# Performance work log

Measured on AMD Instinct MI355X. Metric: run time of the kernel, lower is better.

The kernel has to match this reference:

```python
import jax, jax.numpy as jnp
import numpy as np


def _pairwise_sq_dist(x, y):
    # x: [B, N, 3], y: [B, M, 3] -> P: [B, N, M] squared Euclidean distances
    xx = jnp.sum(x * x, axis=-1)                      # [B, N]
    yy = jnp.sum(y * y, axis=-1)                      # [B, M]
    zz = jnp.einsum('bnd,bmd->bnm', x, y)             # [B, N, M]
    return xx[:, :, None] + yy[:, None, :] - 2.0 * zz


def setup_inputs() -> dict:
    key = jax.random.key(0)
    k1, k2 = jax.random.split(key)
    B, K = 8, 8192
    adv_pc = jax.random.normal(k1, (B, K, 3), dtype=jnp.float32)
    ori_pc = jax.random.normal(k2, (B, K, 3), dtype=jnp.float32)
    weights = jnp.ones((B,), dtype=jnp.float32)
    return {"adv_pc": adv_pc, "ori_pc": ori_pc, "weights": weights}


def reference(adv_pc, ori_pc, weights):
    # P = pairwise_dist(gts=ori_pc, preds=adv_pc): [B, N_ori, N_adv]
    P = _pairwise_sq_dist(ori_pc, adv_pc)
    # method='adv2ori': loss1 = max over adv points of min over ori points
    loss1 = jnp.max(jnp.min(P, axis=1), axis=1)       # [B]
    loss = loss1 * weights
    return jnp.mean(loss)                             # batch_avg=True
```

## Files before the change

kernel.cpp:

```cpp
#include <hip/hip_runtime.h>


#define KPTS 8192
#define BATCH 8
#define NSPLIT 8
#define RBLK (KPTS / NSPLIT)
#define TSLICE (RBLK / 32)
#define CBLK 512
#define MCHUNK (KPTS / CBLK)

typedef _Float16 half8 __attribute__((ext_vector_type(8)));
typedef float f32x16 __attribute__((ext_vector_type(16)));

__device__ __forceinline__ float min16acc(float rm, const f32x16 c) {
    float u0 = fminf(fminf(c[0],  c[1]),  c[2]);
    float u1 = fminf(fminf(c[3],  c[4]),  c[5]);
    float u2 = fminf(fminf(c[6],  c[7]),  c[8]);
    float u3 = fminf(fminf(c[9],  c[10]), c[11]);
    float u4 = fminf(fminf(c[12], c[13]), c[14]);
    float u5 = fminf(fminf(u0, u1), c[15]);
    float u6 = fminf(fminf(u2, u3), u4);
    return fminf(fminf(u5, u6), rm);
}

__global__ __launch_bounds__(256) void hausdorff(const float* __restrict__ adv,
                                                 const float* __restrict__ ori,
                                                 float* __restrict__ part,
                                                 float* __restrict__ out) {
    __shared__ _Float16 sA[(TSLICE + 1) * 512];

    const int bid  = blockIdx.x;
    const int b    = bid >> 7;
    const int mc   = (bid >> 3) & (MCHUNK - 1);
    const int ns   = bid & 7;
    const int tid  = threadIdx.x;
    const int lane = tid & 63;
    const int wv   = tid >> 6;
    const int r    = lane & 31;
    const int hk   = lane >> 5;

    if (bid == 0 && tid == 0) out[0] = 0.0f;

    const _Float16 Z = (_Float16)0.0f, ONE = (_Float16)1.0f;

    const float* advb = adv + (size_t)b * KPTS * 3;
    const int m0 = mc * CBLK + wv * 128 + r;
    half8 bf0, bf1, bf2, bf3;
    float aa0, aa1, aa2, aa3;
#pragma unroll
    for (int i = 0; i < 4; ++i) {
        const int m = m0 + 32 * i;
        float ax = advb[3 * m], ay = advb[3 * m + 1], az = advb[3 * m + 2];
        float aa = ax * ax + ay * ay + az * az;
        float tx = -2.f * ax, ty = -2.f * ay, tz = -2.f * az;
        _Float16 bx = (_Float16)tx, by = (_Float16)ty, bz = (_Float16)tz;
        _Float16 cx = (_Float16)(tx - (float)bx);
        _Float16 cy = (_Float16)(ty - (float)by);
        _Float16 cz = (_Float16)(tz - (float)bz);
        half8 h0 = {bx, by, bz, cx, cy, cz, bx, by};
        half8 h1 = {bz, ONE, ONE, Z, Z, Z, Z, Z};
        half8 bi = hk ? h1 : h0;
        if (i == 0) { bf0 = bi; aa0 = aa; }
        else if (i == 1) { bf1 = bi; aa1 = aa; }
        else if (i == 2) { bf2 = bi; aa2 = aa; }
        else { bf3 = bi; aa3 = aa; }
    }

    const float* orib = ori + ((size_t)b * KPTS + (size_t)ns * RBLK) * 3;
#pragma unroll
    for (int i = 0; i < 4; ++i) {
        const int rr = tid + i * 256;
        const float* op = orib + (size_t)rr * 3;
        float x = op[0], y = op[1], z = op[2];
        float oo = x * x + y * y + z * z;
        _Float16 hx = (_Float16)x, hy = (_Float16)y, hz = (_Float16)z;
        _Float16 lx = (_Float16)(x - (float)hx);
        _Float16 ly = (_Float16)(y - (float)hy);
        _Float16 lz = (_Float16)(z - (float)hz);
        _Float16 oh = (_Float16)oo;
        _Float16 ol = (_Float16)(oo - (float)oh);
        half8 a0 = {hx, hy, hz, hx, hy, hz, lx, ly};
        half8 a1 = {lz, oh, ol, Z, Z, Z, Z, Z};
        const int off = ((rr >> 5) << 9) + ((rr & 31) << 3);
        *(half8*)(&sA[off])       = a0;
        *(half8*)(&sA[off + 256]) = a1;
    }
    __syncthreads();

    f32x16 zc;
#pragma unroll
    for (int i = 0; i < 16; ++i) zc[i] = 0.0f;

    float rm0 = __builtin_huge_valf(), rm1 = __builtin_huge_valf();
    float rm2 = __builtin_huge_valf(), rm3 = __builtin_huge_valf();

    const _Float16* apl = sA + lane * 8;
    half8 af = *(const half8*)apl;

    for (int t = 0; t < TSLICE; ++t) {
        half8 afn = *(const half8*)(apl + (size_t)(t + 1) * 512);

        f32x16 d0, d1, d2, d3;
        asm("v_mfma_f32_32x32x16_f16 %0, %4, %5, %9\n\t"
            "v_mfma_f32_32x32x16_f16 %1, %4, %6, %9\n\t"
            "v_mfma_f32_32x32x16_f16 %2, %4, %7, %9\n\t"
            "v_mfma_f32_32x32x16_f16 %3, %4, %8, %9\n\t"
            "s_nop 7\n\ts_nop 7\n\ts_nop 7\n\ts_nop 7"
            : "=&v"(d0), "=&v"(d1), "=&v"(d2), "=&v"(d3)
            : "v"(af), "v"(bf0), "v"(bf1), "v"(bf2), "v"(bf3), "v"(zc));

        rm0 = min16acc(rm0, d0);
        rm1 = min16acc(rm1, d1);
        rm2 = min16acc(rm2, d2);
        rm3 = min16acc(rm3, d3);
        af = afn;
    }

    rm0 = fminf(rm0, __shfl_xor(rm0, 32, 64));
    rm1 = fminf(rm1, __shfl_xor(rm1, 32, 64));
    rm2 = fminf(rm2, __shfl_xor(rm2, 32, 64));
    rm3 = fminf(rm3, __shfl_xor(rm3, 32, 64));

    float* p = part + ((size_t)ns * BATCH + b) * KPTS;
    if (hk == 0) {
        p[m0]      = fmaxf(rm0 + aa0, 0.0f);
        p[m0 + 32] = fmaxf(rm1 + aa1, 0.0f);
        p[m0 + 64] = fmaxf(rm2 + aa2, 0.0f);
        p[m0 + 96] = fmaxf(rm3 + aa3, 0.0f);
    }
}

__global__ __launch_bounds__(1024) void reduceB(const float* __restrict__ part,
                                                const float* __restrict__ w,
                                                float* __restrict__ out) {
    const int b = blockIdx.x;
    const int tid = threadIdx.x;

    float mx = 0.0f;
#pragma unroll
    for (int h = 0; h < 2; ++h) {
        const int c4 = tid + h * 1024;
        float4 v[NSPLIT];
#pragma unroll
        for (int s = 0; s < NSPLIT; ++s)
            v[s] = *(const float4*)(part + ((size_t)s * BATCH + b) * KPTS + (size_t)c4 * 4);
        float4 mn = v[0];
#pragma unroll
        for (int s = 1; s < NSPLIT; ++s) {
            mn.x = fminf(mn.x, v[s].x); mn.y = fminf(mn.y, v[s].y);
            mn.z = fminf(mn.z, v[s].z); mn.w = fminf(mn.w, v[s].w);
        }
        mx = fmaxf(mx, fmaxf(fmaxf(mn.x, mn.y), fmaxf(mn.z, mn.w)));
    }

#pragma unroll
    for (int off = 32; off; off >>= 1)
        mx = fmaxf(mx, __shfl_xor(mx, off, 64));

    __shared__ float red[16];
    if ((tid & 63) == 0) red[tid >> 6] = mx;
    __syncthreads();
    if (tid == 0) {
        float m2 = red[0];
#pragma unroll
        for (int i = 1; i < 16; ++i) m2 = fmaxf(m2, red[i]);
        atomicAdd(out, m2 * w[b] * (1.0f / BATCH));
    }
}

extern "C" void kernel_launch(void* const* d_in, const int* in_sizes, int n_in,
                              void* d_out, int out_size, void* d_ws, size_t ws_size,
                              hipStream_t stream) {
    const float* adv = (const float*)d_in[0];
    const float* ori = (const float*)d_in[1];
    const float* w   = (const float*)d_in[2];
    float* out = (float*)d_out;
    float* part = (float*)d_ws;

    hausdorff<<<BATCH * MCHUNK * NSPLIT, 256, 0, stream>>>(adv, ori, part, out);
    reduceB<<<BATCH, 1024, 0, stream>>>((const float*)part, w, out);
}
```

Measured before the change: 78.69 us.

## Software-pipeline MFMA tiles with v_min3 reductions in the Hausdorff kernel

Restructures the inner loop so each iteration issues the MFMAs for the next tile while the previous tile's 16 accumulator values are folded into running minima. It adds a prologue and epilogue and fully unrolls the loop. The min reductions now use inline v_min3_f32 instead of chained fminf, and the kernel requests 4 blocks per CU through launch bounds. This is meant to hide MFMA latency and the padding s_nops behind VALU work, at the cost of more registers. It also relies on the toolchain or hardware to handle MFMA-to-VALU read hazards that the old explicit nops covered.

```diff
diff --git a/kernel.cpp b/kernel.cpp
--- a/kernel.cpp
+++ b/kernel.cpp
@@ -12,21 +12,39 @@
 typedef _Float16 half8 __attribute__((ext_vector_type(8)));
 typedef float f32x16 __attribute__((ext_vector_type(16)));
 
-__device__ __forceinline__ float min16acc(float rm, const f32x16 c) {
-    float u0 = fminf(fminf(c[0],  c[1]),  c[2]);
-    float u1 = fminf(fminf(c[3],  c[4]),  c[5]);
-    float u2 = fminf(fminf(c[6],  c[7]),  c[8]);
-    float u3 = fminf(fminf(c[9],  c[10]), c[11]);
-    float u4 = fminf(fminf(c[12], c[13]), c[14]);
-    float u5 = fminf(fminf(u0, u1), c[15]);
-    float u6 = fminf(fminf(u2, u3), u4);
-    return fminf(fminf(u5, u6), rm);
-}
-
-__global__ __launch_bounds__(256) void hausdorff(const float* __restrict__ adv,
-                                                 const float* __restrict__ ori,
-                                                 float* __restrict__ part,
-                                                 float* __restrict__ out) {
+#define FOLD17(rm, c)                                                         \
+    do {                                                                      \
+        float t0_, t1_, t2_, t3_, t4_, t5_, t6_, o_;                          \
+        asm volatile(                                                         \
+            "v_min3_f32 %0, %8, %9, %10\n\t"                                  \
+            "v_min3_f32 %1, %11, %12, %13\n\t"                                \
+            "v_min3_f32 %2, %14, %15, %16\n\t"                                \
+            "v_min3_f32 %3, %17, %18, %19\n\t"                                \
+            "v_min3_f32 %4, %20, %21, %22\n\t"                                \
+            "v_min3_f32 %5, %23, %24, %0\n\t"                                 \
+            "v_min3_f32 %6, %1, %2, %3\n\t"                                   \
+            "v_min3_f32 %7, %4, %5, %6"                                       \
+            : "=&v"(t0_), "=&v"(t1_), "=&v"(t2_), "=&v"(t3_), "=&v"(t4_),     \
+              "=&v"(t5_), "=v"(t6_), "=v"(o_)                                 \
+            : "v"((c)[0]), "v"((c)[1]), "v"((c)[2]), "v"((c)[3]),             \
+              "v"((c)[4]), "v"((c)[5]), "v"((c)[6]), "v"((c)[7]),             \
+              "v"((c)[8]), "v"((c)[9]), "v"((c)[10]), "v"((c)[11]),           \
+              "v"((c)[12]), "v"((c)[13]), "v"((c)[14]), "v"((c)[15]),         \
+              "v"(rm));                                                       \
+        (rm) = o_;                                                            \
+    } while (0)
+
+#define MFMA2(d_a, d_b, af_, bfa, bfb, zc_)                                   \
+    asm volatile(                                                             \
+        "v_mfma_f32_32x32x16_f16 %0, %2, %3, %5\n\t"                          \
+        "v_mfma_f32_32x32x16_f16 %1, %2, %4, %5"                              \
+        : "=&v"(d_a), "=&v"(d_b)                                              \
+        : "v"(af_), "v"(bfa), "v"(bfb), "v"(zc_))
+
+__global__ __launch_bounds__(256, 4) void hausdorff(const float* __restrict__ adv,
+                                                    const float* __restrict__ ori,
+                                                    float* __restrict__ part,
+                                                    float* __restrict__ out) {
     __shared__ _Float16 sA[(TSLICE + 1) * 512];
 
     const int bid  = blockIdx.x;
@@ -95,26 +113,35 @@
     float rm2 = __builtin_huge_valf(), rm3 = __builtin_huge_valf();
 
     const _Float16* apl = sA + lane * 8;
+
     half8 af = *(const half8*)apl;
-
-    for (int t = 0; t < TSLICE; ++t) {
-        half8 afn = *(const half8*)(apl + (size_t)(t + 1) * 512);
-
-        f32x16 d0, d1, d2, d3;
-        asm("v_mfma_f32_32x32x16_f16 %0, %4, %5, %9\n\t"
-            "v_mfma_f32_32x32x16_f16 %1, %4, %6, %9\n\t"
-            "v_mfma_f32_32x32x16_f16 %2, %4, %7, %9\n\t"
-            "v_mfma_f32_32x32x16_f16 %3, %4, %8, %9\n\t"
-            "s_nop 7\n\ts_nop 7\n\ts_nop 7\n\ts_nop 7"
-            : "=&v"(d0), "=&v"(d1), "=&v"(d2), "=&v"(d3)
-            : "v"(af), "v"(bf0), "v"(bf1), "v"(bf2), "v"(bf3), "v"(zc));
-
-        rm0 = min16acc(rm0, d0);
-        rm1 = min16acc(rm1, d1);
-        rm2 = min16acc(rm2, d2);
-        rm3 = min16acc(rm3, d3);
+    f32x16 d0, d1, d2, d3;
+    asm volatile(
+        "v_mfma_f32_32x32x16_f16 %0, %4, %5, %9\n\t"
+        "v_mfma_f32_32x32x16_f16 %1, %4, %6, %9\n\t"
+        "v_mfma_f32_32x32x16_f16 %2, %4, %7, %9\n\t"
+        "v_mfma_f32_32x32x16_f16 %3, %4, %8, %9\n\t"
+        "s_nop 7\n\ts_nop 7"
+        : "=&v"(d0), "=&v"(d1), "=&v"(d2), "=&v"(d3)
+        : "v"(af), "v"(bf0), "v"(bf1), "v"(bf2), "v"(bf3), "v"(zc));
+
+#pragma unroll
+    for (int t = 1; t < TSLICE; ++t) {
+        half8 afn = *(const half8*)(apl + (size_t)t * 512);
+        FOLD17(rm0, d0);
+        FOLD17(rm1, d1);
+        MFMA2(d0, d1, afn, bf0, bf1, zc);
+        FOLD17(rm2, d2);
+        FOLD17(rm3, d3);
+        MFMA2(d2, d3, afn, bf2, bf3, zc);
         af = afn;
     }
+
+    asm volatile("s_nop 7\n\ts_nop 7" ::: );
+    FOLD17(rm0, d0);
+    FOLD17(rm1, d1);
+    FOLD17(rm2, d2);
+    FOLD17(rm3, d3);
 
     rm0 = fminf(rm0, __shfl_xor(rm0, 32, 64));
     rm1 = fminf(rm1, __shfl_xor(rm1, 32, 64));
```

New measurement: 77.11 us. -2.0%, faster.
